# Optimization experiments

Measured on AMD Instinct MI355X. Metric: run time of the kernel, lower is better.

The kernel has to match this reference:

```python
import jax, jax.numpy as jnp
import numpy as np

HEADS = 8
WSZ = 8
DIM_KEY = 32
DIM_VALUE = 32
DIM = 256
EPS = 1e-5


def setup_inputs() -> dict:
    key = jax.random.key(0)
    ks = jax.random.split(key, 8)
    B, C, H, W = 16, DIM, 128, 128
    inner_k = DIM_KEY * HEADS
    inner_v = DIM_VALUE * HEADS
    x = jax.random.normal(ks[0], (B, C, H, W), dtype=jnp.float32)
    g = jnp.ones((C,), dtype=jnp.float32)
    b = jnp.zeros((C,), dtype=jnp.float32)
    wq = jax.random.normal(ks[1], (inner_k, C), dtype=jnp.float32) * (C ** -0.5)
    wk = jax.random.normal(ks[2], (inner_k, C), dtype=jnp.float32) * (C ** -0.5)
    wv = jax.random.normal(ks[3], (inner_v, C), dtype=jnp.float32) * (C ** -0.5)
    local_w = jax.random.normal(ks[4], (inner_v, inner_v, 3, 3), dtype=jnp.float32) * ((inner_v * 9) ** -0.5)
    local_b = jnp.zeros((inner_v,), dtype=jnp.float32)
    out_w = jax.random.normal(ks[5], (C, inner_v), dtype=jnp.float32) * (inner_v ** -0.5)
    out_b = jnp.zeros((C,), dtype=jnp.float32)
    return {"x": x, "g": g, "b": b, "wq": wq, "wk": wk, "wv": wv,
            "local_w": local_w, "local_b": local_b, "out_w": out_w, "out_b": out_b}


def _to_windows(t, heads, wsz):
    # [B, heads*d, H, W] -> [B*X*Y, heads, wsz*wsz, d]
    B, Ch, H, W = t.shape
    d = Ch // heads
    X, Y = H // wsz, W // wsz
    t = t.reshape(B, heads, d, X, wsz, Y, wsz)
    t = t.transpose(0, 3, 5, 1, 4, 6, 2)  # B X Y heads w1 w2 d
    return t.reshape(B * X * Y, heads, wsz * wsz, d)


def _from_windows(t, B, heads, wsz, H, W):
    X, Y = H // wsz, W // wsz
    d = t.shape[-1]
    t = t.reshape(B, X, Y, heads, wsz, wsz, d)
    t = t.transpose(0, 3, 6, 1, 4, 2, 5)  # B heads d X w1 Y w2
    return t.reshape(B, heads * d, H, W)


def reference(x, g, b, wq, wk, wv, local_w, local_b, out_w, out_b):
    B, C, H, W = x.shape
    # ChanLayerNorm over channel dim (biased var)
    mean = jnp.mean(x, axis=1, keepdims=True)
    var = jnp.var(x, axis=1, keepdims=True)
    xn = (x - mean) / jnp.sqrt(var + EPS) * g[None, :, None, None] + b[None, :, None, None]
    # 1x1 conv projections as einsum
    q = jnp.einsum('oc,bchw->bohw', wq, xn)
    k = jnp.einsum('oc,bchw->bohw', wk, xn)
    v = jnp.einsum('oc,bchw->bohw', wv, xn)
    # local interactive 3x3 conv on v
    local_out = jax.lax.conv_general_dilated(
        v, local_w, window_strides=(1, 1), padding='SAME',
        dimension_numbers=('NCHW', 'OIHW', 'NCHW')) + local_b[None, :, None, None]
    # windowed attention
    qw = _to_windows(q, HEADS, WSZ)
    kw = _to_windows(k, HEADS, WSZ)
    vw = _to_windows(v, HEADS, WSZ)
    scale = DIM_KEY ** -0.5
    dots = jnp.einsum('whid,whjd->whij', qw, kw) * scale
    attn = jax.nn.softmax(dots, axis=-1)
    out = jnp.einsum('whij,whjd->whid', attn, vw)
    out = _from_windows(out, B, HEADS, WSZ, H, W)
    out = out + local_out
    # to_out 1x1 conv with bias
    return jnp.einsum('oc,bchw->bohw', out_w, out) + out_b[None, :, None, None]
```

## Files before the change

### kernel.cpp

```cpp
#include <hip/hip_runtime.h>

typedef __attribute__((ext_vector_type(8))) short short8;
typedef __attribute__((ext_vector_type(4))) float f32x4;

#define DEV static __device__ __forceinline__

typedef __attribute__((address_space(1))) void GVoid;
typedef __attribute__((address_space(3))) void LVoid;

DEV unsigned short f2bf(float f) {
  unsigned u = __builtin_bit_cast(unsigned, f);
  u += 0x7fffu + ((u >> 16) & 1u);
  return (unsigned short)(u >> 16);
}
DEV float bf2f(unsigned short h) {
  unsigned u = ((unsigned)h) << 16;
  return __builtin_bit_cast(float, u);
}
DEV void cp16(void* lds_uniform_base, const void* gsrc) {
  __builtin_amdgcn_global_load_lds((GVoid*)gsrc, (LVoid*)lds_uniform_base, 16, 0, 0);
}

DEV void xcd_remap(int& mb, int& nb) {
  const int gx = gridDim.x;
  const int p = blockIdx.x + gx * blockIdx.y;
  const int nwg = gx * gridDim.y;
  const int q = nwg >> 3;
  const int L = (p & 7) * q + (p >> 3);
  mb = L % gx;
  nb = L / gx;
}

__global__ __launch_bounds__(256) void setup_kernel(
    const float* __restrict__ wq, const float* __restrict__ wk, const float* __restrict__ wv,
    const float* __restrict__ lw, const float* __restrict__ ow,
    unsigned short* __restrict__ wqkvb, unsigned short* __restrict__ w2b,
    unsigned short* __restrict__ woutb, unsigned short* __restrict__ zp)
{
  int i = blockIdx.x * 256 + threadIdx.x;
  if (i < 196608) {
    float f = (i < 65536) ? wq[i] : (i < 131072) ? wk[i - 65536] : wv[i - 131072];
    wqkvb[i] = f2bf(f);
  } else if (i < 786432) {
    int j = i - 196608;
    int co = j / 2304;
    int r = j - co * 2304;
    int tap = r >> 8;
    int ci = r & 255;
    w2b[j] = f2bf(lw[(co * 256 + ci) * 9 + tap]);
  } else if (i < 851968) {
    int j = i - 786432;
    woutb[j] = f2bf(ow[j]);
  } else if (i < 852096) {
    zp[i - 851968] = 0;
  }
}

__global__ __launch_bounds__(256) void ln_kernel(
    const float* __restrict__ x, const float* __restrict__ gw,
    const float* __restrict__ bw, unsigned short* __restrict__ xn)
{
  const int t = threadIdx.x;
  const int p = blockIdx.x * 256 + t;
  const int b = p >> 14;
  const int pix = p & 16383;
  const int h = pix >> 7;
  const int w = pix & 127;
  const float* xp = x + ((size_t)b << 22) + pix;

  float sum = 0.f, ss = 0.f;
#pragma unroll 8
  for (int c = 0; c < 256; ++c) {
    float f = xp[(size_t)c << 14];
    sum += f;
    ss += f * f;
  }
  float mean = sum * (1.f / 256.f);
  float var = ss * (1.f / 256.f) - mean * mean;
  float inv = rsqrtf(var + 1e-5f);

  const int pw = ((b * 16 + (h >> 3)) * 16 + (w >> 3)) * 64 + (h & 7) * 8 + (w & 7);
  unsigned short* op = xn + (size_t)pw * 256;
#pragma unroll 2
  for (int c = 0; c < 256; c += 4) {
    float f0 = xp[(size_t)(c + 0) << 14];
    float f1 = xp[(size_t)(c + 1) << 14];
    float f2 = xp[(size_t)(c + 2) << 14];
    float f3 = xp[(size_t)(c + 3) << 14];
    float v0 = (f0 - mean) * inv * gw[c + 0] + bw[c + 0];
    float v1 = (f1 - mean) * inv * gw[c + 1] + bw[c + 1];
    float v2 = (f2 - mean) * inv * gw[c + 2] + bw[c + 2];
    float v3 = (f3 - mean) * inv * gw[c + 3] + bw[c + 3];
    unsigned long long pk = (unsigned long long)f2bf(v0) |
                            ((unsigned long long)f2bf(v1) << 16) |
                            ((unsigned long long)f2bf(v2) << 32) |
                            ((unsigned long long)f2bf(v3) << 48);
    *(unsigned long long*)(op + c) = pk;
  }
}

DEV void mfma_tile(const unsigned short* As, const unsigned short* Bs,
                   int wm, int wn, int l15, int quad, f32x4 (&acc)[4][4])
{
#pragma unroll
  for (int ks = 0; ks < 2; ++ks) {
    short8 a[4], b[4];
#pragma unroll
    for (int i = 0; i < 4; ++i)
      a[i] = *(const short8*)(As + (wm + i * 16 + l15) * 64 + ks * 32 + quad * 8);
#pragma unroll
    for (int j = 0; j < 4; ++j)
      b[j] = *(const short8*)(Bs + (wn + j * 16 + l15) * 64 + ks * 32 + quad * 8);
#pragma unroll
    for (int i = 0; i < 4; ++i)
#pragma unroll
      for (int j = 0; j < 4; ++j)
        acc[i][j] = __builtin_amdgcn_mfma_f32_16x16x32_bf16(a[i], b[j], acc[i][j], 0, 0, 0);
  }
}

__global__ __launch_bounds__(256) void qkv_gemm(
    const unsigned short* __restrict__ wqkvb, const unsigned short* __restrict__ xn,
    unsigned short* __restrict__ qb, unsigned short* __restrict__ kb,
    unsigned short* __restrict__ vb)
{
  __shared__ __align__(16) unsigned short As[128 * 64];
  __shared__ __align__(16) unsigned short Bs[128 * 64];
  const int tid = threadIdx.x;
  const int lane = tid & 63;
  const int wave = tid >> 6;
  const int l15 = lane & 15;
  const int quad = lane >> 4;
  const int wm = (wave >> 1) * 64;
  const int wn = (wave & 1) * 64;
  const int sub = tid & 7;
  const int row0 = tid >> 3;
  int mb, nb;
  xcd_remap(mb, nb);
  const int m0 = mb * 128;
  const int n0 = nb * 128;

  f32x4 acc[4][4];
  f32x4 zero = {0.f, 0.f, 0.f, 0.f};
#pragma unroll
  for (int i = 0; i < 4; ++i)
#pragma unroll
    for (int j = 0; j < 4; ++j) acc[i][j] = zero;

  for (int kt = 0; kt < 4; ++kt) {
    const int k0 = kt * 64;
#pragma unroll
    for (int it = 0; it < 4; ++it) {
      const int row = it * 32 + row0;
      cp16(As + (size_t)(it * 256 + wave * 64) * 8,
           wqkvb + (size_t)(m0 + row) * 256 + k0 + sub * 8);
      cp16(Bs + (size_t)(it * 256 + wave * 64) * 8,
           xn + (size_t)(n0 + row) * 256 + k0 + sub * 8);
    }
    __syncthreads();
    mfma_tile(As, Bs, wm, wn, l15, quad, acc);
    __syncthreads();
  }

  unsigned short* ob = (m0 < 256) ? qb : (m0 < 512) ? kb : vb;
  const int chb = (m0 & 255) + wm;
#pragma unroll
  for (int i = 0; i < 4; ++i) {
    const int ch = chb + i * 16 + quad * 4;
#pragma unroll
    for (int j = 0; j < 4; ++j) {
      const int n = n0 + wn + j * 16 + l15;
      unsigned long long pk = (unsigned long long)f2bf(acc[i][j][0]) |
                              ((unsigned long long)f2bf(acc[i][j][1]) << 16) |
                              ((unsigned long long)f2bf(acc[i][j][2]) << 32) |
                              ((unsigned long long)f2bf(acc[i][j][3]) << 48);
      *(unsigned long long*)(ob + (size_t)n * 256 + ch) = pk;
    }
  }
}

__global__ __launch_bounds__(128) void attn_kernel(
    const unsigned short* __restrict__ qb, const unsigned short* __restrict__ kb,
    const unsigned short* __restrict__ vb, unsigned short* __restrict__ attnb)
{
  __shared__ float4 ks4[2][64][9];
  __shared__ float4 vs4[2][64][9];
  const int tid = threadIdx.x;
  const int tok = tid & 63;
  const int hs = tid >> 6;
  const int win = blockIdx.x >> 2;
  const int head = (blockIdx.x & 3) * 2 + hs;
  const size_t base = (size_t)(win * 64 + tok) * 256 + head * 32;

  float qf[32];
  {
    const uint4* qp4 = (const uint4*)(qb + base);
    const uint4* kp4 = (const uint4*)(kb + base);
    const uint4* vp4 = (const uint4*)(vb + base);
#pragma unroll
    for (int i = 0; i < 4; ++i) {
      uint4 u = qp4[i];
      qf[8 * i + 0] = bf2f((unsigned short)(u.x & 0xffff));
      qf[8 * i + 1] = bf2f((unsigned short)(u.x >> 16));
      qf[8 * i + 2] = bf2f((unsigned short)(u.y & 0xffff));
      qf[8 * i + 3] = bf2f((unsigned short)(u.y >> 16));
      qf[8 * i + 4] = bf2f((unsigned short)(u.z & 0xffff));
      qf[8 * i + 5] = bf2f((unsigned short)(u.z >> 16));
      qf[8 * i + 6] = bf2f((unsigned short)(u.w & 0xffff));
      qf[8 * i + 7] = bf2f((unsigned short)(u.w >> 16));
    }
#pragma unroll
    for (int i = 0; i < 4; ++i) {
      uint4 u = kp4[i];
      float4 f0, f1;
      f0.x = bf2f((unsigned short)(u.x & 0xffff));
      f0.y = bf2f((unsigned short)(u.x >> 16));
      f0.z = bf2f((unsigned short)(u.y & 0xffff));
      f0.w = bf2f((unsigned short)(u.y >> 16));
      f1.x = bf2f((unsigned short)(u.z & 0xffff));
      f1.y = bf2f((unsigned short)(u.z >> 16));
      f1.z = bf2f((unsigned short)(u.w & 0xffff));
      f1.w = bf2f((unsigned short)(u.w >> 16));
      ks4[hs][tok][2 * i] = f0;
      ks4[hs][tok][2 * i + 1] = f1;
      uint4 v = vp4[i];
      float4 g0, g1;
      g0.x = bf2f((unsigned short)(v.x & 0xffff));
      g0.y = bf2f((unsigned short)(v.x >> 16));
      g0.z = bf2f((unsigned short)(v.y & 0xffff));
      g0.w = bf2f((unsigned short)(v.y >> 16));
      g1.x = bf2f((unsigned short)(v.z & 0xffff));
      g1.y = bf2f((unsigned short)(v.z >> 16));
      g1.z = bf2f((unsigned short)(v.w & 0xffff));
      g1.w = bf2f((unsigned short)(v.w >> 16));
      vs4[hs][tok][2 * i] = g0;
      vs4[hs][tok][2 * i + 1] = g1;
    }
  }
  __syncthreads();

  float dots[64];
#pragma unroll
  for (int j = 0; j < 64; ++j) {
    float d = 0.f;
#pragma unroll
    for (int c4 = 0; c4 < 8; ++c4) {
      float4 kk = ks4[hs][j][c4];
      d += qf[4 * c4 + 0] * kk.x + qf[4 * c4 + 1] * kk.y +
           qf[4 * c4 + 2] * kk.z + qf[4 * c4 + 3] * kk.w;
    }
    dots[j] = d * 0.17677669529663688f;
  }
  float mx = -1e30f;
#pragma unroll
  for (int j = 0; j < 64; ++j) mx = fmaxf(mx, dots[j]);
  float s = 0.f;
#pragma unroll
  for (int j = 0; j < 64; ++j) {
    float e = __expf(dots[j] - mx);
    dots[j] = e;
    s += e;
  }
  const float rs = 1.f / s;

  float of[32];
#pragma unroll
  for (int c = 0; c < 32; ++c) of[c] = 0.f;
#pragma unroll
  for (int j = 0; j < 64; ++j) {
    const float p = dots[j];
#pragma unroll
    for (int c4 = 0; c4 < 8; ++c4) {
      float4 vv = vs4[hs][j][c4];
      of[4 * c4 + 0] += p * vv.x;
      of[4 * c4 + 1] += p * vv.y;
      of[4 * c4 + 2] += p * vv.z;
      of[4 * c4 + 3] += p * vv.w;
    }
  }
  uint4* op4 = (uint4*)(attnb + base);
#pragma unroll
  for (int i = 0; i < 4; ++i) {
    uint4 o;
    o.x = (unsigned)f2bf(of[8 * i + 0] * rs) | ((unsigned)f2bf(of[8 * i + 1] * rs) << 16);
    o.y = (unsigned)f2bf(of[8 * i + 2] * rs) | ((unsigned)f2bf(of[8 * i + 3] * rs) << 16);
    o.z = (unsigned)f2bf(of[8 * i + 4] * rs) | ((unsigned)f2bf(of[8 * i + 5] * rs) << 16);
    o.w = (unsigned)f2bf(of[8 * i + 6] * rs) | ((unsigned)f2bf(of[8 * i + 7] * rs) << 16);
    op4[i] = o;
  }
}

__global__ __launch_bounds__(256) void conv_gemm(
    const unsigned short* __restrict__ w2b, const unsigned short* __restrict__ vbuf,
    const unsigned short* __restrict__ attnb, const float* __restrict__ lbias,
    const unsigned short* __restrict__ zp, unsigned short* __restrict__ sumb)
{
  __shared__ __align__(16) unsigned short As[128 * 64];
  __shared__ __align__(16) unsigned short Bs[128 * 64];
  const int tid = threadIdx.x;
  const int lane = tid & 63;
  const int wave = tid >> 6;
  const int l15 = lane & 15;
  const int quad = lane >> 4;
  const int wm = (wave >> 1) * 64;
  const int wn = (wave & 1) * 64;
  const int sub = tid & 7;
  const int row0 = tid >> 3;
  int mb, nb;
  xcd_remap(mb, nb);
  const int m0 = mb * 128;
  const int n0 = nb * 128;

  int bi[4], hh[4], ww[4];
#pragma unroll
  for (int it = 0; it < 4; ++it) {
    int n = n0 + it * 32 + row0;
    int b = n >> 14;
    int r = n & 16383;
    int Xw = r >> 10;
    int r2 = r & 1023;
    int Yw = r2 >> 6;
    int t2 = r2 & 63;
    bi[it] = b;
    hh[it] = Xw * 8 + (t2 >> 3);
    ww[it] = Yw * 8 + (t2 & 7);
  }

  f32x4 acc[4][4];
  f32x4 zero = {0.f, 0.f, 0.f, 0.f};
#pragma unroll
  for (int i = 0; i < 4; ++i)
#pragma unroll
    for (int j = 0; j < 4; ++j) acc[i][j] = zero;

  for (int tap = 0; tap < 9; ++tap) {
    const int dy = tap / 3 - 1;
    const int dx = tap - (tap / 3) * 3 - 1;
    const unsigned short* bp[4];
    int bstep[4];
#pragma unroll
    for (int it = 0; it < 4; ++it) {
      int h2 = hh[it] + dy, w2 = ww[it] + dx;
      bool ok = ((unsigned)h2 < 128u) && ((unsigned)w2 < 128u);
      int nn = ((bi[it] * 16 + (h2 >> 3)) * 16 + (w2 >> 3)) * 64 + (h2 & 7) * 8 + (w2 & 7);
      bp[it] = ok ? (vbuf + (size_t)nn * 256 + sub * 8) : (zp + sub * 8);
      bstep[it] = ok ? 64 : 0;
    }
    for (int cc = 0; cc < 4; ++cc) {
#pragma unroll
      for (int it = 0; it < 4; ++it) {
        cp16(As + (size_t)(it * 256 + wave * 64) * 8,
             w2b + ((size_t)(m0 + it * 32 + row0) * 9 + tap) * 256 + cc * 64 + sub * 8);
        cp16(Bs + (size_t)(it * 256 + wave * 64) * 8, bp[it] + cc * bstep[it]);
      }
      __syncthreads();
      mfma_tile(As, Bs, wm, wn, l15, quad, acc);
      __syncthreads();
    }
  }

#pragma unroll
  for (int i = 0; i < 4; ++i) {
    const int ch = m0 + wm + i * 16 + quad * 4;
    const float b0 = lbias[ch + 0], b1 = lbias[ch + 1], b2 = lbias[ch + 2], b3 = lbias[ch + 3];
#pragma unroll
    for (int j = 0; j < 4; ++j) {
      const int n = n0 + wn + j * 16 + l15;
      const unsigned* ap = (const unsigned*)(attnb + (size_t)n * 256 + ch);
      unsigned a0 = ap[0], a1 = ap[1];
      float r0 = acc[i][j][0] + b0 + bf2f((unsigned short)(a0 & 0xffff));
      float r1 = acc[i][j][1] + b1 + bf2f((unsigned short)(a0 >> 16));
      float r2 = acc[i][j][2] + b2 + bf2f((unsigned short)(a1 & 0xffff));
      float r3 = acc[i][j][3] + b3 + bf2f((unsigned short)(a1 >> 16));
      unsigned long long pk = (unsigned long long)f2bf(r0) |
                              ((unsigned long long)f2bf(r1) << 16) |
                              ((unsigned long long)f2bf(r2) << 32) |
                              ((unsigned long long)f2bf(r3) << 48);
      *(unsigned long long*)(sumb + (size_t)n * 256 + ch) = pk;
    }
  }
}

__global__ __launch_bounds__(256) void out_gemm(
    const unsigned short* __restrict__ woutb, const unsigned short* __restrict__ sumb,
    const float* __restrict__ obias, float* __restrict__ out)
{
  __shared__ __align__(16) unsigned short As[128 * 64];
  __shared__ __align__(16) unsigned short Bs[128 * 64];
  const int tid = threadIdx.x;
  const int lane = tid & 63;
  const int wave = tid >> 6;
  const int l15 = lane & 15;
  const int quad = lane >> 4;
  const int wm = (wave >> 1) * 64;
  const int wn = (wave & 1) * 64;
  const int sub = tid & 7;
  const int row0 = tid >> 3;
  int mb, nb;
  xcd_remap(mb, nb);
  const int m0 = mb * 128;
  const int n0 = nb * 128;

  f32x4 acc[4][4];
  f32x4 zero = {0.f, 0.f, 0.f, 0.f};
#pragma unroll
  for (int i = 0; i < 4; ++i)
#pragma unroll
    for (int j = 0; j < 4; ++j) acc[i][j] = zero;

  for (int kt = 0; kt < 4; ++kt) {
    const int k0 = kt * 64;
#pragma unroll
    for (int it = 0; it < 4; ++it) {
      const int row = it * 32 + row0;
      cp16(As + (size_t)(it * 256 + wave * 64) * 8,
           woutb + (size_t)(m0 + row) * 256 + k0 + sub * 8);
      cp16(Bs + (size_t)(it * 256 + wave * 64) * 8,
           sumb + (size_t)(n0 + row) * 256 + k0 + sub * 8);
    }
    __syncthreads();
    mfma_tile(As, Bs, wm, wn, l15, quad, acc);
    __syncthreads();
  }

  int bb4[4], hw4[4];
#pragma unroll
  for (int j = 0; j < 4; ++j) {
    int n = n0 + wn + j * 16 + l15;
    int b = n >> 14;
    int r = n & 16383;
    int Xw = r >> 10;
    int r2 = r & 1023;
    int Yw = r2 >> 6;
    int t2 = r2 & 63;
    bb4[j] = b;
    hw4[j] = (Xw * 8 + (t2 >> 3)) * 128 + Yw * 8 + (t2 & 7);
  }
#pragma unroll
  for (int i = 0; i < 4; ++i) {
    const int mb2 = m0 + wm + i * 16 + quad * 4;
    const float o0 = obias[mb2 + 0], o1 = obias[mb2 + 1], o2 = obias[mb2 + 2], o3 = obias[mb2 + 3];
#pragma unroll
    for (int j = 0; j < 4; ++j) {
      float* o = out + ((size_t)(bb4[j] * 256 + mb2) << 14) + hw4[j];
      o[0] = acc[i][j][0] + o0;
      o[(size_t)1 << 14] = acc[i][j][1] + o1;
      o[(size_t)2 << 14] = acc[i][j][2] + o2;
      o[(size_t)3 << 14] = acc[i][j][3] + o3;
    }
  }
}

extern "C" void kernel_launch(void* const* d_in, const int* in_sizes, int n_in,
                              void* d_out, int out_size, void* d_ws, size_t ws_size,
                              hipStream_t stream)
{
  const float* x  = (const float*)d_in[0];
  const float* g  = (const float*)d_in[1];
  const float* bb = (const float*)d_in[2];
  const float* wq = (const float*)d_in[3];
  const float* wk = (const float*)d_in[4];
  const float* wv = (const float*)d_in[5];
  const float* lw = (const float*)d_in[6];
  const float* lb = (const float*)d_in[7];
  const float* ow = (const float*)d_in[8];
  const float* ob = (const float*)d_in[9];
  float* out = (float*)d_out;

  char* ws = (char*)d_ws;
  unsigned short* wqkvb = (unsigned short*)(ws + 0);
  unsigned short* w2b   = (unsigned short*)(ws + 393216);
  unsigned short* woutb = (unsigned short*)(ws + 1572864);
  unsigned short* zp    = (unsigned short*)(ws + 1703936);
  const size_t BUF0 = 1704192;

  int nimg = 16;
  while (nimg > 1 && BUF0 + 4ull * (size_t)nimg * 8388608ull > ws_size) nimg >>= 1;
  const size_t bufB = (size_t)nimg * 8388608ull;
  unsigned short* xnb = (unsigned short*)(ws + BUF0);
  unsigned short* qb  = (unsigned short*)(ws + BUF0 + bufB);
  unsigned short* kb  = (unsigned short*)(ws + BUF0 + 2 * bufB);
  unsigned short* vb  = (unsigned short*)(ws + BUF0 + 3 * bufB);
  unsigned short* attnb = xnb;
  unsigned short* sumb  = qb;

  setup_kernel<<<3329, 256, 0, stream>>>(wq, wk, wv, lw, ow, wqkvb, w2b, woutb, zp);

  const int nchunk = 16 / nimg;
  const int Nc = nimg * 16384;
  for (int c = 0; c < nchunk; ++c) {
    const float* xc = x + (size_t)c * nimg * 256 * 16384;
    float* oc = out + (size_t)c * nimg * 256 * 16384;
    ln_kernel<<<Nc / 256, 256, 0, stream>>>(xc, g, bb, xnb);
    qkv_gemm<<<dim3(6, Nc / 128), 256, 0, stream>>>(wqkvb, xnb, qb, kb, vb);
    attn_kernel<<<(Nc / 64) * 4, 128, 0, stream>>>(qb, kb, vb, attnb);
    conv_gemm<<<dim3(2, Nc / 128), 256, 0, stream>>>(w2b, vb, attnb, lb, zp, sumb);
    out_gemm<<<dim3(2, Nc / 128), 256, 0, stream>>>(woutb, sumb, ob, oc);
  }
}
```

Baseline: 1.867 ms.

## Swizzle GEMM LDS tiles with XOR and use fp16 dot2 in window attention

Three GEMM kernels (qkv, local conv, output) now load 16-byte chunks into LDS with an XOR swizzle on the k-chunk index, and mfma_tile reads with the matching swizzle. The aim is to remove LDS bank conflicts on the 128-byte row stride. Separately, the attention kernel stores K and transposed V in LDS as fp16 and computes QK^T and PV with packed fp16 dot2 instructions, halving LDS footprint and cutting FMA count. This lowers attention precision to fp16 (including the softmax probabilities) and changes unroll factors.

```diff
diff --git a/kernel.cpp b/kernel.cpp
--- a/kernel.cpp
+++ b/kernel.cpp
@@ -2,6 +2,7 @@
 
 typedef __attribute__((ext_vector_type(8))) short short8;
 typedef __attribute__((ext_vector_type(4))) float f32x4;
+typedef __attribute__((ext_vector_type(2))) _Float16 h2;
 
 #define DEV static __device__ __forceinline__
 
@@ -20,6 +21,10 @@
 DEV void cp16(void* lds_uniform_base, const void* gsrc) {
   __builtin_amdgcn_global_load_lds((GVoid*)gsrc, (LVoid*)lds_uniform_base, 16, 0, 0);
 }
+DEV float fdot2(h2 a, h2 b, float c) {
+  return __builtin_amdgcn_fdot2(a, b, c, false);
+}
+DEV h2 bch2(float f) { return __builtin_bit_cast(h2, f); }
 
 DEV void xcd_remap(int& mb, int& nb) {
   const int gx = gridDim.x;
@@ -102,15 +107,17 @@
 DEV void mfma_tile(const unsigned short* As, const unsigned short* Bs,
                    int wm, int wn, int l15, int quad, f32x4 (&acc)[4][4])
 {
+  const int sx = l15 & 7;
 #pragma unroll
   for (int ks = 0; ks < 2; ++ks) {
+    const int sl = ((ks * 4 + quad) ^ sx) * 8;
     short8 a[4], b[4];
 #pragma unroll
     for (int i = 0; i < 4; ++i)
-      a[i] = *(const short8*)(As + (wm + i * 16 + l15) * 64 + ks * 32 + quad * 8);
+      a[i] = *(const short8*)(As + (wm + i * 16 + l15) * 64 + sl);
 #pragma unroll
     for (int j = 0; j < 4; ++j)
-      b[j] = *(const short8*)(Bs + (wn + j * 16 + l15) * 64 + ks * 32 + quad * 8);
+      b[j] = *(const short8*)(Bs + (wn + j * 16 + l15) * 64 + sl);
 #pragma unroll
     for (int i = 0; i < 4; ++i)
 #pragma unroll
@@ -135,6 +142,7 @@
   const int wn = (wave & 1) * 64;
   const int sub = tid & 7;
   const int row0 = tid >> 3;
+  const int ssub = sub ^ (row0 & 7);
   int mb, nb;
   xcd_remap(mb, nb);
   const int m0 = mb * 128;
@@ -153,9 +161,9 @@
     for (int it = 0; it < 4; ++it) {
       const int row = it * 32 + row0;
       cp16(As + (size_t)(it * 256 + wave * 64) * 8,
-           wqkvb + (size_t)(m0 + row) * 256 + k0 + sub * 8);
+           wqkvb + (size_t)(m0 + row) * 256 + k0 + ssub * 8);
       cp16(Bs + (size_t)(it * 256 + wave * 64) * 8,
-           xn + (size_t)(n0 + row) * 256 + k0 + sub * 8);
+           xn + (size_t)(n0 + row) * 256 + k0 + ssub * 8);
     }
     __syncthreads();
     mfma_tile(As, Bs, wm, wn, l15, quad, acc);
@@ -183,8 +191,8 @@
     const unsigned short* __restrict__ qb, const unsigned short* __restrict__ kb,
     const unsigned short* __restrict__ vb, unsigned short* __restrict__ attnb)
 {
-  __shared__ float4 ks4[2][64][9];
-  __shared__ float4 vs4[2][64][9];
+  __shared__ __align__(16) _Float16 ks2[2][64][40];
+  __shared__ __align__(16) _Float16 vs2[2][32][64];
   const int tid = threadIdx.x;
   const int tok = tid & 63;
   const int hs = tid >> 6;
@@ -192,7 +200,7 @@
   const int head = (blockIdx.x & 3) * 2 + hs;
   const size_t base = (size_t)(win * 64 + tok) * 256 + head * 32;
 
-  float qf[32];
+  h2 q2[16];
   {
     const uint4* qp4 = (const uint4*)(qb + base);
     const uint4* kp4 = (const uint4*)(kb + base);
@@ -200,54 +208,49 @@
 #pragma unroll
     for (int i = 0; i < 4; ++i) {
       uint4 u = qp4[i];
-      qf[8 * i + 0] = bf2f((unsigned short)(u.x & 0xffff));
-      qf[8 * i + 1] = bf2f((unsigned short)(u.x >> 16));
-      qf[8 * i + 2] = bf2f((unsigned short)(u.y & 0xffff));
-      qf[8 * i + 3] = bf2f((unsigned short)(u.y >> 16));
-      qf[8 * i + 4] = bf2f((unsigned short)(u.z & 0xffff));
-      qf[8 * i + 5] = bf2f((unsigned short)(u.z >> 16));
-      qf[8 * i + 6] = bf2f((unsigned short)(u.w & 0xffff));
-      qf[8 * i + 7] = bf2f((unsigned short)(u.w >> 16));
+      unsigned uu[4] = {u.x, u.y, u.z, u.w};
+#pragma unroll
+      for (int w = 0; w < 4; ++w) {
+        h2 p;
+        p.x = (_Float16)bf2f((unsigned short)(uu[w] & 0xffff));
+        p.y = (_Float16)bf2f((unsigned short)(uu[w] >> 16));
+        q2[i * 4 + w] = p;
+      }
     }
 #pragma unroll
     for (int i = 0; i < 4; ++i) {
       uint4 u = kp4[i];
-      float4 f0, f1;
-      f0.x = bf2f((unsigned short)(u.x & 0xffff));
-      f0.y = bf2f((unsigned short)(u.x >> 16));
-      f0.z = bf2f((unsigned short)(u.y & 0xffff));
-      f0.w = bf2f((unsigned short)(u.y >> 16));
-      f1.x = bf2f((unsigned short)(u.z & 0xffff));
-      f1.y = bf2f((unsigned short)(u.z >> 16));
-      f1.z = bf2f((unsigned short)(u.w & 0xffff));
-      f1.w = bf2f((unsigned short)(u.w >> 16));
-      ks4[hs][tok][2 * i] = f0;
-      ks4[hs][tok][2 * i + 1] = f1;
+      unsigned uu[4] = {u.x, u.y, u.z, u.w};
+#pragma unroll
+      for (int w = 0; w < 4; ++w) {
+        int c = 2 * (i * 4 + w);
+        ks2[hs][tok][c + 0] = (_Float16)bf2f((unsigned short)(uu[w] & 0xffff));
+        ks2[hs][tok][c + 1] = (_Float16)bf2f((unsigned short)(uu[w] >> 16));
+      }
       uint4 v = vp4[i];
-      float4 g0, g1;
-      g0.x = bf2f((unsigned short)(v.x & 0xffff));
-      g0.y = bf2f((unsigned short)(v.x >> 16));
-      g0.z = bf2f((unsigned short)(v.y & 0xffff));
-      g0.w = bf2f((unsigned short)(v.y >> 16));
-      g1.x = bf2f((unsigned short)(v.z & 0xffff));
-      g1.y = bf2f((unsigned short)(v.z >> 16));
-      g1.z = bf2f((unsigned short)(v.w & 0xffff));
-      g1.w = bf2f((unsigned short)(v.w >> 16));
-      vs4[hs][tok][2 * i] = g0;
-      vs4[hs][tok][2 * i + 1] = g1;
+      unsigned vv[4] = {v.x, v.y, v.z, v.w};
+#pragma unroll
+      for (int w = 0; w < 4; ++w) {
+        int c = 2 * (i * 4 + w);
+        vs2[hs][c + 0][tok] = (_Float16)bf2f((unsigned short)(vv[w] & 0xffff));
+        vs2[hs][c + 1][tok] = (_Float16)bf2f((unsigned short)(vv[w] >> 16));
+      }
     }
   }
   __syncthreads();
 
   float dots[64];
-#pragma unroll
+#pragma unroll 4
   for (int j = 0; j < 64; ++j) {
+    const float4* kr = (const float4*)ks2[hs][j];
     float d = 0.f;
 #pragma unroll
-    for (int c4 = 0; c4 < 8; ++c4) {
-      float4 kk = ks4[hs][j][c4];
-      d += qf[4 * c4 + 0] * kk.x + qf[4 * c4 + 1] * kk.y +
-           qf[4 * c4 + 2] * kk.z + qf[4 * c4 + 3] * kk.w;
+    for (int qq = 0; qq < 4; ++qq) {
+      float4 raw = kr[qq];
+      d = fdot2(q2[4 * qq + 0], bch2(raw.x), d);
+      d = fdot2(q2[4 * qq + 1], bch2(raw.y), d);
+      d = fdot2(q2[4 * qq + 2], bch2(raw.z), d);
+      d = fdot2(q2[4 * qq + 3], bch2(raw.w), d);
     }
     dots[j] = d * 0.17677669529663688f;
   }
@@ -263,21 +266,31 @@
   }
   const float rs = 1.f / s;
 
+  h2 p2[32];
+#pragma unroll
+  for (int jp = 0; jp < 32; ++jp) {
+    h2 p;
+    p.x = (_Float16)dots[2 * jp];
+    p.y = (_Float16)dots[2 * jp + 1];
+    p2[jp] = p;
+  }
+
   float of[32];
-#pragma unroll
-  for (int c = 0; c < 32; ++c) of[c] = 0.f;
-#pragma unroll
-  for (int j = 0; j < 64; ++j) {
-    const float p = dots[j];
-#pragma unroll
-    for (int c4 = 0; c4 < 8; ++c4) {
-      float4 vv = vs4[hs][j][c4];
-      of[4 * c4 + 0] += p * vv.x;
-      of[4 * c4 + 1] += p * vv.y;
-      of[4 * c4 + 2] += p * vv.z;
-      of[4 * c4 + 3] += p * vv.w;
-    }
-  }
+#pragma unroll 4
+  for (int c = 0; c < 32; ++c) {
+    const float4* vr = (const float4*)vs2[hs][c];
+    float o = 0.f;
+#pragma unroll
+    for (int qq = 0; qq < 8; ++qq) {
+      float4 raw = vr[qq];
+      o = fdot2(p2[4 * qq + 0], bch2(raw.x), o);
+      o = fdot2(p2[4 * qq + 1], bch2(raw.y), o);
+      o = fdot2(p2[4 * qq + 2], bch2(raw.z), o);
+      o = fdot2(p2[4 * qq + 3], bch2(raw.w), o);
+    }
+    of[c] = o;
+  }
+
   uint4* op4 = (uint4*)(attnb + base);
 #pragma unroll
   for (int i = 0; i < 4; ++i) {
@@ -306,6 +319,7 @@
   const int wn = (wave & 1) * 64;
   const int sub = tid & 7;
   const int row0 = tid >> 3;
+  const int ssub = sub ^ (row0 & 7);
   int mb, nb;
   xcd_remap(mb, nb);
   const int m0 = mb * 128;
@@ -340,17 +354,17 @@
     int bstep[4];
 #pragma unroll
     for (int it = 0; it < 4; ++it) {
-      int h2 = hh[it] + dy, w2 = ww[it] + dx;
-      bool ok = ((unsigned)h2 < 128u) && ((unsigned)w2 < 128u);
-      int nn = ((bi[it] * 16 + (h2 >> 3)) * 16 + (w2 >> 3)) * 64 + (h2 & 7) * 8 + (w2 & 7);
-      bp[it] = ok ? (vbuf + (size_t)nn * 256 + sub * 8) : (zp + sub * 8);
+      int h2_ = hh[it] + dy, w2_ = ww[it] + dx;
+      bool ok = ((unsigned)h2_ < 128u) && ((unsigned)w2_ < 128u);
+      int nn = ((bi[it] * 16 + (h2_ >> 3)) * 16 + (w2_ >> 3)) * 64 + (h2_ & 7) * 8 + (w2_ & 7);
+      bp[it] = ok ? (vbuf + (size_t)nn * 256 + ssub * 8) : (zp + ssub * 8);
       bstep[it] = ok ? 64 : 0;
     }
     for (int cc = 0; cc < 4; ++cc) {
 #pragma unroll
       for (int it = 0; it < 4; ++it) {
         cp16(As + (size_t)(it * 256 + wave * 64) * 8,
-             w2b + ((size_t)(m0 + it * 32 + row0) * 9 + tap) * 256 + cc * 64 + sub * 8);
+             w2b + ((size_t)(m0 + it * 32 + row0) * 9 + tap) * 256 + cc * 64 + ssub * 8);
         cp16(Bs + (size_t)(it * 256 + wave * 64) * 8, bp[it] + cc * bstep[it]);
       }
       __syncthreads();
@@ -396,6 +410,7 @@
   const int wn = (wave & 1) * 64;
   const int sub = tid & 7;
   const int row0 = tid >> 3;
+  const int ssub = sub ^ (row0 & 7);
   int mb, nb;
   xcd_remap(mb, nb);
   const int m0 = mb * 128;
@@ -414,9 +429,9 @@
     for (int it = 0; it < 4; ++it) {
       const int row = it * 32 + row0;
       cp16(As + (size_t)(it * 256 + wave * 64) * 8,
-           woutb + (size_t)(m0 + row) * 256 + k0 + sub * 8);
+           woutb + (size_t)(m0 + row) * 256 + k0 + ssub * 8);
       cp16(Bs + (size_t)(it * 256 + wave * 64) * 8,
-           sumb + (size_t)(n0 + row) * 256 + k0 + sub * 8);
+           sumb + (size_t)(n0 + row) * 256 + k0 + ssub * 8);
     }
     __syncthreads();
     mfma_tile(As, Bs, wm, wn, l15, quad, acc);
```

Measured after the change: 1.751 ms. 6.2% less time.
